# Performance work log

Hardware: AMD Instinct MI355X
Metric: run time of the kernel (lower is better)

Reference implementation:

```python
import jax, jax.numpy as jnp
import numpy as np

N, B, E, H, D, L, NT = 30000, 16, 60000, 128, 64, 2, 5


def _build_graph():
    rng = np.random.default_rng(0)
    ng = N // B
    row = rng.integers(0, N, size=E)
    g = row // ng
    col = g * ng + rng.integers(0, ng, size=E)  # bonds stay within a graph
    order = np.argsort(g, kind='stable')        # sort bonds by graph id
    row, col = row[order], col[order]
    edge_index = np.stack([row, col]).astype(np.int32)
    # bond graph: bonds adjacent iff they share an atom (vectorized _build_bond_graph)
    atoms = np.concatenate([row, col])
    bonds = np.concatenate([np.arange(E), np.arange(E)])
    o2 = np.argsort(atoms, kind='stable')
    sb = bonds[o2]
    counts = np.bincount(atoms, minlength=N)
    offs = np.concatenate([[0], np.cumsum(counts)[:-1]])
    sq = counts * counts
    total = int(sq.sum())
    gid = np.repeat(np.arange(N), sq)
    poff = np.concatenate([[0], np.cumsum(sq)[:-1]])
    pos = np.arange(total) - np.repeat(poff, sq)
    c, o = counts[gid], offs[gid]
    ii, jj = pos // c, pos % c
    mask = ii != jj
    bond_edge_index = np.stack([sb[o + ii][mask], sb[o + jj][mask]]).astype(np.int32)
    batch = np.repeat(np.arange(B), ng).astype(np.int32)
    return edge_index, bond_edge_index, batch


def setup_inputs() -> dict:
    edge_index, bond_edge_index, batch = _build_graph()
    key = jax.random.key(0)
    ks = jax.random.split(key, 16)
    s = 0.05
    n = lambda k, shp: jax.random.normal(k, shp, jnp.float32) * s
    return {
        'atom_features': jax.random.normal(ks[0], (N, H), jnp.float32),
        'atom_pos': jax.random.normal(ks[1], (N, 3), jnp.float32),
        'atomic_numbers': jax.random.randint(ks[2], (N,), 1, 20, jnp.int32),
        'batch': jnp.asarray(batch),
        'edge_index': jnp.asarray(edge_index),
        'bond_edge_index': jnp.asarray(bond_edge_index),
        'iw1': n(ks[3], (2 * H, D)), 'ib1': jnp.zeros((D,), jnp.float32),
        'iw2': n(ks[4], (D, D)), 'ib2': jnp.zeros((D,), jnp.float32),
        'emb': n(ks[5], (L, NT, D)),
        'mw1': n(ks[6], (L, 3 * D, D)), 'mb1': jnp.zeros((L, D), jnp.float32),
        'mw2': n(ks[7], (L, D, D)), 'mb2': jnp.zeros((L, D), jnp.float32),
        'uw1': n(ks[8], (L, 2 * D, D)), 'ub1': jnp.zeros((L, D), jnp.float32),
        'uw2': n(ks[9], (L, D, D)), 'ub2': jnp.zeros((L, D), jnp.float32),
        'num_graphs': B,
    }


def reference(atom_features, atom_pos, iw1, ib1, iw2, ib2, emb, mw1, mb1, mw2, mb2,
              uw1, ub1, uw2, ub2, atomic_numbers, batch, edge_index, bond_edge_index,
              num_graphs):
    row, col = edge_index
    hi, hj = atom_features[row], atom_features[col]  # [E, H] gathers
    # bond_init MLP
    x = jax.nn.silu(jnp.concatenate([hi, hj], -1) @ iw1 + ib1) @ iw2 + ib2  # [E, D]
    # _classify_bonds: cosine-similarity thresholds (order matters, matches torch)
    ni = jnp.maximum(jnp.linalg.norm(hi, axis=-1), 1e-8)
    nj = jnp.maximum(jnp.linalg.norm(hj, axis=-1), 1e-8)
    sim = jnp.sum(hi * hj, -1) / (ni * nj)
    bt = jnp.where(sim > 0.8, 1, 0)
    bt = jnp.where(sim > 0.9, 2, bt)
    bt = jnp.where(sim < 0.3, 3, bt)
    src, dst = bond_edge_index  # x_j = x[src], x_i = x[dst]; aggregate at dst
    nb = x.shape[0]
    deg = jax.ops.segment_sum(jnp.ones(src.shape, jnp.float32), dst, num_segments=nb)
    denom = jnp.maximum(deg, 1.0)[:, None]  # PyG mean aggr: 0 for isolated nodes
    for l in range(mw1.shape[0]):
        te = emb[l][bt]  # [E, D] bond-type embedding
        msg_in = jnp.concatenate([x[dst], x[src], te[dst]], -1)  # [BE, 3D]
        msg = jax.nn.silu(msg_in @ mw1[l] + mb1[l]) @ mw2[l] + mb2[l]
        aggr = jax.ops.segment_sum(msg, dst, num_segments=nb) / denom
        upd_in = jnp.concatenate([aggr, x], -1)
        x = x + jax.nn.silu(upd_in @ uw1[l] + ub1[l]) @ uw2[l] + ub2[l]
    # pooling: edges are sorted by graph, so repeat_interleave == batch[row]
    bond_batch = batch[row]
    cnt = jax.ops.segment_sum(jnp.ones((nb,), jnp.float32), bond_batch, num_segments=num_graphs)
    gfeat = jax.ops.segment_sum(x, bond_batch, num_segments=num_graphs) / jnp.maximum(cnt, 1.0)[:, None]
    return x, gfeat
```

## Files before the change

### kernel.cpp

```cpp
#include <hip/hip_runtime.h>
#include <cstdint>
#include <cstddef>

#define HDIM 128
#define DDIM 64
#define NTYPES 5
#define NGRAPHS 16
#define EPB 64
#define SCAP 1024

typedef __attribute__((ext_vector_type(8))) short short8;
typedef __attribute__((ext_vector_type(4))) float f32x4;

static __device__ __forceinline__ short8 as_s8(uint4 u) {
    return __builtin_bit_cast(short8, u);
}

static __device__ __forceinline__ float silu_f(float v) {
    return v * __builtin_amdgcn_rcpf(1.0f + __expf(-v));
}

static __device__ __forceinline__ float4 ld4(const float* p) {
    return *reinterpret_cast<const float4*>(p);
}

static __device__ __forceinline__ void st4(float* p, float4 v) {
    *reinterpret_cast<float4*>(p) = v;
}

static __device__ __forceinline__ float4 add4(float4 a, float4 b) {
    return make_float4(a.x + b.x, a.y + b.y, a.z + b.z, a.w + b.w);
}
// ... 26 lines not shown
    a.x = __uint_as_float(u.x << 16);
    a.y = __uint_as_float(u.x & 0xFFFF0000u);
    a.z = __uint_as_float(u.y << 16);
    a.w = __uint_as_float(u.y & 0xFFFF0000u);
    b.x = __uint_as_float(u.z << 16);
    b.y = __uint_as_float(u.z & 0xFFFF0000u);
    b.z = __uint_as_float(u.w << 16);
    b.w = __uint_as_float(u.w & 0xFFFF0000u);
}

static __device__ __forceinline__ void hilo8(const float* f, uint4& h, uint4& lo) {
    h = pack8(f);
    float4 a, b;
    unpack8(h, a, b);
    lo.x = cvtpk(f[0] - a.x, f[1] - a.y);
    lo.y = cvtpk(f[2] - a.z, f[3] - a.w);
    lo.z = cvtpk(f[4] - b.x, f[5] - b.y);
    lo.w = cvtpk(f[6] - b.z, f[7] - b.w);
}

static __device__ __forceinline__ int xcd_logical_block() {
    int chunk = (int)(gridDim.x >> 3);
    return (int)(blockIdx.x & 7) * chunk + (int)(blockIdx.x >> 3);
}

__global__ void __launch_bounds__(256) count_k(const int* __restrict__ bdst,
                                               int* __restrict__ cnt, int BE) {
    int i = blockIdx.x * 256 + threadIdx.x;
    if (i < BE)
        __hip_atomic_fetch_add(&cnt[bdst[i]], 1, __ATOMIC_RELAXED, __HIP_MEMORY_SCOPE_AGENT);
}

__global__ void __launch_bounds__(256) bsum_k(const int* __restrict__ cnt,
                                              int* __restrict__ bsum, int E) {
    __shared__ int red[256];
    int t = threadIdx.x;
    int i = blockIdx.x * 256 + t;
    red[t] = (i < E) ? cnt[i] : 0;
    __syncthreads();
    #pragma unroll
    for (int off = 128; off > 0; off >>= 1) {
        if (t < off) red[t] += red[t + off];
        __syncthreads();
    }
    if (t == 0) bsum[blockIdx.x] = red[0];
}

__global__ void __launch_bounds__(1024) bscan_k(const int* __restrict__ bsum,
                                                int* __restrict__ bpre, int NB) {
    __shared__ int sh[1024];
    int t = threadIdx.x;
    int v0 = (t < NB) ? bsum[t] : 0;
    sh[t] = v0;
// ... 21 lines not shown
        int v = (t >= off) ? sh[t - off] : 0;
        __syncthreads();
        sh[t] += v;
        __syncthreads();
    }
    int ex = sh[t] - v0 + bpre[blockIdx.x];
    if (i < E) { offs[i] = ex; cursor[i] = ex; }
    if (i == E - 1) offs[E] = ex + v0;
}

__global__ void __launch_bounds__(256) scatter_k(const int* __restrict__ bsrc,
                                                 const int* __restrict__ bdst,
                                                 int* __restrict__ cursor,
                                                 int* __restrict__ srclist, int BE) {
    int i = blockIdx.x * 256 + threadIdx.x;
    if (i < BE) {
        int d = bdst[i];
        int p = __hip_atomic_fetch_add(&cursor[d], 1, __ATOMIC_RELAXED,
                                       __HIP_MEMORY_SCOPE_AGENT);
        srclist[p] = bsrc[i];
    }
}

__global__ void __launch_bounds__(64) prep_k(const float* __restrict__ emb,
                                             const float* __restrict__ mw1,
                                             const float* __restrict__ mb1,
                                             const float* __restrict__ mw2,
                                             const float* __restrict__ mb2,
                                             const float* __restrict__ uw1,
                                             const float* __restrict__ uw2,
                                             const float* __restrict__ iw2,
                                             const float* __restrict__ iw1,
                                             float* __restrict__ tt,
                                             float* __restrict__ b2u,
                                             uint4* __restrict__ fw2u,
                                             uint4* __restrict__ fu1b,
                                             uint4* __restrict__ fu2,
                                             uint4* __restrict__ fp,
                                             uint4* __restrict__ fiw2,
                                             uint4* __restrict__ fp0,
                                             uint4* __restrict__ fiw1) {
    int b = blockIdx.x;
    int l = threadIdx.x;
    if (b < 10) {
        int ll = b / NTYPES, t = b % NTYPES;
        const float* embl = emb + (size_t)ll * NTYPES * DDIM + (size_t)t * DDIM;
        const float* w1 = mw1 + (size_t)ll * 192 * DDIM;
        float s = mb1[ll * DDIM + l];
        #pragma unroll 8
        for (int k = 0; k < DDIM; ++k)
            s = fmaf(embl[k], w1[(HDIM + k) * DDIM + l], s);
        tt[(size_t)b * DDIM + l] = s;
        return;
    }
    if (b < 12) {
        int ll = b - 10;
        const float* u1 = uw1 + (size_t)ll * 128 * DDIM;
        float s = 0.f;
        #pragma unroll 8
        for (int t = 0; t < DDIM; ++t)
            s = fmaf(mb2[ll * DDIM + t], u1[(size_t)t * DDIM + l], s);
        b2u[ll * DDIM + l] = s;
        return;
    }
    int pb = b - 12;
    int mat = pb >> 3, jt = (pb >> 1) & 3, ks = pb & 1;
// ... 20 lines not shown
            case 3:  src = uw1 + 128 * 64 + 64 * 64;         dst = fu1b + 1024; break;
            case 4:  src = uw2;                              dst = fu2;         break;
            case 5:  src = uw2 + 4096;                       dst = fu2 + 1024;  break;
            case 6:  src = mw1 + (size_t)192 * 64;           dst = fp;          break;
            case 7:  src = mw1 + (size_t)192 * 64 + 64 * 64; dst = fp + 1024;   break;
            case 8:  src = iw2;                              dst = fiw2;        break;
            case 9:  src = mw1;                              dst = fp0;         break;
            case 10: src = mw1 + (size_t)64 * 64;            dst = fp0 + 1024;  break;
            case 11: src = iw1;                              dst = fiw1;        break;
            case 12: src = iw1 + (size_t)64 * 64;            dst = fiw1 + 1024; break;
            case 13: src = iw1 + (size_t)128 * 64;           dst = fiw1 + 2048; break;
            default: src = iw1 + (size_t)192 * 64;           dst = fiw1 + 3072; break;
        }
        #pragma unroll
        for (int i = 0; i < 8; ++i) f[i] = src[(size_t)(k0 + i) * DDIM + j];
    }
    uint4 h, lo;
    hilo8(f, h, lo);
    size_t di = ((size_t)(jt * 2 + ks) * 64 + l) * 2;
    dst[di] = h;
    dst[di + 1] = lo;
}

static __device__ __forceinline__ int slotIdx(int row, int slot) {
    return row * 8 + (slot ^ (row & 7));
}
static __device__ __forceinline__ int slotIdx16(int row, int slot) {
    return row * 16 + (slot ^ (row & 7));
}

static __device__ __forceinline__ short8 ldFragA(const uint4* buf, int rowBase, int lane, int ks) {
    int row = rowBase + (lane & 15);
    int slot = ks * 4 + (lane >> 4);
    return as_s8(buf[slotIdx(row, slot)]);
}
static __device__ __forceinline__ short8 ldFragA16(const uint4* buf, int rowBase, int lane, int slot0) {
    int row = rowBase + (lane & 15);
    int slot = slot0 + (lane >> 4);
    return as_s8(buf[slotIdx16(row, slot)]);
}

static __device__ __forceinline__ void loadB(const uint4* __restrict__ frag, int jt, int lane,
                                             short8& h0, short8& h1, short8& l0, short8& l1) {
    const uint4* p0 = frag + ((size_t)(jt * 2 + 0) * 64 + lane) * 2;
    const uint4* p1 = frag + ((size_t)(jt * 2 + 1) * 64 + lane) * 2;
    h0 = as_s8(p0[0]); l0 = as_s8(p0[1]);
// ... 12 lines not shown
    acc = __builtin_amdgcn_mfma_f32_16x16x32_bf16(al0, bh0, acc, 0, 0, 0);
    acc = __builtin_amdgcn_mfma_f32_16x16x32_bf16(al1, bh1, acc, 0, 0, 0);
    acc = __builtin_amdgcn_mfma_f32_16x16x32_bf16(ah0, bl0, acc, 0, 0, 0);
    acc = __builtin_amdgcn_mfma_f32_16x16x32_bf16(ah1, bl1, acc, 0, 0, 0);
    return acc;
}

static __device__ __forceinline__ f32x4 gemm_tile16(const uint4* Ahi, const uint4* Alo,
        int rowBase, int lane, int sb,
        short8 bh0, short8 bh1, short8 bl0, short8 bl1, f32x4 acc) {
    short8 ah0 = ldFragA16(Ahi, rowBase, lane, sb + 0);
    short8 ah1 = ldFragA16(Ahi, rowBase, lane, sb + 4);
    short8 al0 = ldFragA16(Alo, rowBase, lane, sb + 0);
    short8 al1 = ldFragA16(Alo, rowBase, lane, sb + 4);
    acc = __builtin_amdgcn_mfma_f32_16x16x32_bf16(ah0, bh0, acc, 0, 0, 0);
    acc = __builtin_amdgcn_mfma_f32_16x16x32_bf16(ah1, bh1, acc, 0, 0, 0);
    acc = __builtin_amdgcn_mfma_f32_16x16x32_bf16(al0, bh0, acc, 0, 0, 0);
    acc = __builtin_amdgcn_mfma_f32_16x16x32_bf16(al1, bh1, acc, 0, 0, 0);
    acc = __builtin_amdgcn_mfma_f32_16x16x32_bf16(ah0, bl0, acc, 0, 0, 0);
    acc = __builtin_amdgcn_mfma_f32_16x16x32_bf16(ah1, bl1, acc, 0, 0, 0);
    return acc;
}

__global__ void __launch_bounds__(512) atom_proj_k(
    const float* __restrict__ AF, const uint4* __restrict__ fIw1,
    float* __restrict__ pa, float* __restrict__ qa, float* __restrict__ na, int N) {
    __shared__ uint4 sHi[1024];
    __shared__ uint4 sLo[1024];
    int tid = threadIdx.x;
    int lane = tid & 63;
    int w = __builtin_amdgcn_readfirstlane((int)(tid >> 6));
    int a0 = blockIdx.x * 64;

    {
        int dl = tid >> 3, q = tid & 7;
        int a = a0 + dl;
        bool ok = a < N;
        const float* ar = AF + (size_t)(ok ? a : 0) * HDIM + q * 16;
        float4 v0 = ld4(ar + 0), v1 = ld4(ar + 4), v2 = ld4(ar + 8), v3 = ld4(ar + 12);
        float nrm = v0.x*v0.x + v0.y*v0.y + v0.z*v0.z + v0.w*v0.w
                  + v1.x*v1.x + v1.y*v1.y + v1.z*v1.z + v1.w*v1.w
                  + v2.x*v2.x + v2.y*v2.y + v2.z*v2.z + v2.w*v2.w
                  + v3.x*v3.x + v3.y*v3.y + v3.z*v3.z + v3.w*v3.w;
        nrm += __shfl_xor(nrm, 1, 64);
        nrm += __shfl_xor(nrm, 2, 64);
        nrm += __shfl_xor(nrm, 4, 64);
        if (q == 0 && ok) na[a] = sqrtf(nrm);
        float f0[8] = {v0.x, v0.y, v0.z, v0.w, v1.x, v1.y, v1.z, v1.w};
        float f1[8] = {v2.x, v2.y, v2.z, v2.w, v3.x, v3.y, v3.z, v3.w};
        if (!ok) {
            #pragma unroll
            for (int i = 0; i < 8; ++i) { f0[i] = 0.f; f1[i] = 0.f; }
        }
        uint4 h, l;
        hilo8(f0, h, l);
        int s0 = slotIdx16(dl, q * 2);
// ... 5 lines not shown
    int jt = w & 3;
    const uint4* m0 = fIw1 + ((w < 4) ? 0 : 2048);
    short8 B0h0, B0h1, B0l0, B0l1, B1h0, B1h1, B1l0, B1l1;
    loadB(m0, jt, lane, B0h0, B0h1, B0l0, B0l1);
    loadB(m0 + 1024, jt, lane, B1h0, B1h1, B1l0, B1l1);
    __syncthreads();

    float* dst = (w < 4) ? pa : qa;
    int j = jt * 16 + (lane & 15);
    f32x4 z4 = {0.f, 0.f, 0.f, 0.f};
    #pragma unroll
    for (int rt = 0; rt < 4; ++rt) {
        f32x4 acc = gemm_tile16(sHi, sLo, rt * 16, lane, 0, B0h0, B0h1, B0l0, B0l1, z4);
        acc = gemm_tile16(sHi, sLo, rt * 16, lane, 8, B1h0, B1h1, B1l0, B1l1, acc);
        #pragma unroll
        for (int r = 0; r < 4; ++r) {
            int rowi = rt * 16 + (lane >> 4) * 4 + r;
            int a = a0 + rowi;
            if (a < N) dst[(size_t)a * DDIM + j] = acc[r];
        }
    }
}

__global__ void __launch_bounds__(512, 4) bond_init2_k(
    const float* __restrict__ AF, const int* __restrict__ row, const int* __restrict__ col,
    const float* __restrict__ pa, const float* __restrict__ qa, const float* __restrict__ na,
    const float* __restrict__ b1, const uint4* __restrict__ fW2, const float* __restrict__ b2,
    const uint4* __restrict__ fP0,
    float* __restrict__ x, int* __restrict__ bt,
    float* __restrict__ pd, uint4* __restrict__ ps, int E) {
    __shared__ uint4 sAhi[512];
    __shared__ uint4 sAlo[512];
    __shared__ uint4 sXhi[512];
    __shared__ uint4 sXlo[512];
    int nEB = (E + EPB - 1) / EPB;
    int lb = xcd_logical_block();
    if (lb >= nEB) return;
    int tid = threadIdx.x;
    int lane = tid & 63;
    int w = __builtin_amdgcn_readfirstlane((int)(tid >> 6));
    int e0 = lb * EPB;

    {
        int dl = tid >> 3, q = tid & 7;
        int d = e0 + dl;
        bool ok = d < E;
        int dd = ok ? d : 0;
        int r = row[dd], c = col[dd];
        int jq = q * 8;

        const float* hi = AF + (size_t)r * HDIM + q * 16;
        const float* hj = AF + (size_t)c * HDIM + q * 16;
        float dt = 0.f;
        #pragma unroll
        for (int k = 0; k < 16; k += 4) {
            float4 a4 = ld4(hi + k), b4 = ld4(hj + k);
            dt += a4.x * b4.x + a4.y * b4.y + a4.z * b4.z + a4.w * b4.w;
        }
        dt += __shfl_xor(dt, 1, 64);
        dt += __shfl_xor(dt, 2, 64);
        dt += __shfl_xor(dt, 4, 64);
        if (q == 0 && ok) {
            float nr = fmaxf(na[r], 1e-8f), nc = fmaxf(na[c], 1e-8f);
// ... 25 lines not shown
        uint4 h4, l4;
        hilo8(hv, h4, l4);
        int si = slotIdx(dl, q);
        sAhi[si] = h4; sAlo[si] = l4;
    }
    int jt = w & 3, mh = w >> 2;
    short8 W2h0, W2h1, W2l0, W2l1;
    loadB(fW2, jt, lane, W2h0, W2h1, W2l0, W2l1);
    __syncthreads();

    int rb0 = mh * 32, rb1 = mh * 32 + 16;
    f32x4 z4 = {0.f, 0.f, 0.f, 0.f};
    f32x4 acc0 = gemm_tile(sAhi, sAlo, rb0, lane, W2h0, W2h1, W2l0, W2l1, z4);
    f32x4 acc1 = gemm_tile(sAhi, sAlo, rb1, lane, W2h0, W2h1, W2l0, W2l1, z4);
    int j = jt * 16 + (lane & 15);
    float b2j = b2[j];
    unsigned short* hX = (unsigned short*)sXhi;
    unsigned short* lX = (unsigned short*)sXlo;
    #pragma unroll
    for (int r = 0; r < 4; ++r) {
        int rowi = rb0 + (lane >> 4) * 4 + r;
        int e = e0 + rowi;
        float xn = acc0[r] + b2j;
        if (e < E) x[(size_t)e * DDIM + j] = xn;
        unsigned int hb = bf16r(xn);
        float lov = xn - __uint_as_float(hb << 16);
        int ui = (rowi * 8 + ((j >> 3) ^ (rowi & 7))) * 8 + (j & 7);
        hX[ui] = (unsigned short)hb;
        lX[ui] = (unsigned short)bf16r(lov);
    }
    #pragma unroll
    for (int r = 0; r < 4; ++r) {
        int rowi = rb1 + (lane >> 4) * 4 + r;
        int e = e0 + rowi;
        float xn = acc1[r] + b2j;
        if (e < E) x[(size_t)e * DDIM + j] = xn;
        unsigned int hb = bf16r(xn);
        float lov = xn - __uint_as_float(hb << 16);
        int ui = (rowi * 8 + ((j >> 3) ^ (rowi & 7))) * 8 + (j & 7);
        hX[ui] = (unsigned short)hb;
        lX[ui] = (unsigned short)bf16r(lov);
    }
    __syncthreads();

    const uint4* fPw = (w < 4) ? fP0 : (fP0 + 1024);
    int jp = w & 3;
    short8 Ph0, Ph1, Pl0, Pl1;
    loadB(fPw, jp, lane, Ph0, Ph1, Pl0, Pl1);
    f32x4 q0 = gemm_tile(sXhi, sXlo, 0,  lane, Ph0, Ph1, Pl0, Pl1, z4);
    f32x4 q1 = gemm_tile(sXhi, sXlo, 16, lane, Ph0, Ph1, Pl0, Pl1, z4);
    f32x4 q2 = gemm_tile(sXhi, sXlo, 32, lane, Ph0, Ph1, Pl0, Pl1, z4);
    f32x4 q3 = gemm_tile(sXhi, sXlo, 48, lane, Ph0, Ph1, Pl0, Pl1, z4);
    unsigned short* hA = (unsigned short*)sAhi;
    if (w < 4) {
        int jd = jp * 16 + (lane & 15);
        #pragma unroll
        for (int mt = 0; mt < 4; ++mt) {
            f32x4 qq = (mt == 0) ? q0 : (mt == 1) ? q1 : (mt == 2) ? q2 : q3;
            #pragma unroll
// ... 4 lines not shown
            }
        }
    } else {
        int js = jp * 16 + (lane & 15);
        #pragma unroll
        for (int mt = 0; mt < 4; ++mt) {
            f32x4 qq = (mt == 0) ? q0 : (mt == 1) ? q1 : (mt == 2) ? q2 : q3;
            #pragma unroll
            for (int r = 0; r < 4; ++r) {
                int rowi = mt * 16 + (lane >> 4) * 4 + r;
                int ui = (rowi * 8 + ((js >> 3) ^ (rowi & 7))) * 8 + (js & 7);
                hA[ui] = (unsigned short)bf16r(qq[r]);
            }
        }
    }
    __syncthreads();
    {
        int dl = tid >> 3, q = tid & 7;
        int d = e0 + dl;
        if (d < E) ps[(size_t)d * 8 + q] = sAhi[slotIdx(dl, q)];
    }
}

__global__ void __launch_bounds__(256) proj_k(const float* __restrict__ x,
                                              const float* __restrict__ w1 ,
                                              float* __restrict__ pd, uint4* __restrict__ ps,
                                              int E) {
    int lane = threadIdx.x & 63;
    int w = __builtin_amdgcn_readfirstlane((int)(threadIdx.x >> 6));
    int e = blockIdx.x * EPB + lane;
    bool ok = e < E;
    int eidx = ok ? e : 0;
    int j0 = w * 16;
    const float* xr = x + (size_t)eidx * DDIM;

    float apd[16], aps[16];
    #pragma unroll
    for (int jj = 0; jj < 16; ++jj) { apd[jj] = 0.f; aps[jj] = 0.f; }
    #pragma unroll 2
    for (int c = 0; c < 16; ++c) {
        float4 v = ld4(xr + c * 4);
        float xv[4] = {v.x, v.y, v.z, v.w};
        #pragma unroll
        for (int kk = 0; kk < 4; ++kk) {
            int k = c * 4 + kk;
            const float* wd = w1 + (size_t)k * DDIM + j0;
            const float* wsv = w1 + (size_t)(DDIM + k) * DDIM + j0;
            #pragma unroll
            for (int jj = 0; jj < 16; ++jj) {
                apd[jj] = fmaf(xv[kk], wd[jj], apd[jj]);
                aps[jj] = fmaf(xv[kk], wsv[jj], aps[jj]);
            }
        }
    }
    if (ok) {
        float* pr = pd + (size_t)e * DDIM + j0;
        st4(pr + 0,  make_float4(apd[0],  apd[1],  apd[2],  apd[3]));
        st4(pr + 4,  make_float4(apd[4],  apd[5],  apd[6],  apd[7]));
        st4(pr + 8,  make_float4(apd[8],  apd[9],  apd[10], apd[11]));
        st4(pr + 12, make_float4(apd[12], apd[13], apd[14], apd[15]));
        ps[(size_t)e * 8 + 2 * w + 0] = pack8(aps + 0);
        ps[(size_t)e * 8 + 2 * w + 1] = pack8(aps + 8);
    }
}

__global__ void __launch_bounds__(512, 4) layer_k(
    float* __restrict__ x, const float* __restrict__ pd, const uint4* __restrict__ ps,
    const float* __restrict__ tt_l, const int* __restrict__ bt,
    const int* __restrict__ offs, const int* __restrict__ srclist,
    const int* __restrict__ cnt,
    const uint4* __restrict__ fW2u, const float* __restrict__ b2u,
    const uint4* __restrict__ fU1b, const float* __restrict__ ub1,
    const uint4* __restrict__ fU2, const float* __restrict__ ub2,
    const uint4* __restrict__ fP ,
    float* __restrict__ pdn, uint4* __restrict__ psn, int E,
    const int* __restrict__ erow, const int* __restrict__ gbatch,
    float* __restrict__ gfeat, int doPool) {
    __shared__ uint4 sAhi[512];
    __shared__ uint4 sAlo[512];
    __shared__ uint4 sXhi[512];
    __shared__ uint4 sXlo[512];
    __shared__ float degLDS[64];
    __shared__ int   gidLDS[64];
    __shared__ int   sIdx[SCAP];
    int nEB = (E + EPB - 1) / EPB;
    int lb = xcd_logical_block();
    if (lb >= nEB) return;
    int tid = threadIdx.x;
    int lane = tid & 63;
    int w = __builtin_amdgcn_readfirstlane((int)(tid >> 6));
    int e0 = lb * EPB;
    int pb0 = offs[e0];

    {
        int dl = tid >> 3, q = tid & 7;
        int d = e0 + dl;
        bool ok = d < E;
        int dd = ok ? d : 0;
        int jq = q * 8;
        const float* xr = x + (size_t)dd * DDIM + jq;
        float4 xv0 = ld4(xr + 0), xv1 = ld4(xr + 4);
        int dc = cnt[dd];
        int rAtom = (doPool && ok) ? erow[dd] : 0;
        const float* pr = pd + (size_t)dd * DDIM + jq;
        const float* tp = tt_l + (size_t)bt[dd] * DDIM + jq;
        float4 b0 = add4(ld4(pr + 0), ld4(tp + 0));
        float4 b1 = add4(ld4(pr + 4), ld4(tp + 4));
        int p0v = ok ? offs[d] : pb0, p1v = ok ? offs[d + 1] : pb0;

        int emax = min(e0 + EPB, E);
        int pT = offs[emax] - pb0;
        for (int i = tid; i < pT && i < SCAP; i += 512) sIdx[i] = srclist[pb0 + i];
        __syncthreads();

        float4 s0 = make_float4(0, 0, 0, 0), s1 = s0;
        if (p1v - pb0 <= SCAP) {
            int li = p0v - pb0, le = p1v - pb0;
            for (; li + 4 <= le; li += 4) {
                uint4 u0 = ps[(size_t)sIdx[li + 0] * 8 + q];
                uint4 u1 = ps[(size_t)sIdx[li + 1] * 8 + q];
                uint4 u2 = ps[(size_t)sIdx[li + 2] * 8 + q];
                uint4 u3 = ps[(size_t)sIdx[li + 3] * 8 + q];
                float4 a, b;
                unpack8(u0, a, b);
// ... 28 lines not shown
                silu_acc4(s0, add4(b0, a));
                silu_acc4(s1, add4(b1, b));
                unpack8(u1, a, b);
                silu_acc4(s0, add4(b0, a));
                silu_acc4(s1, add4(b1, b));
                unpack8(u2, a, b);
                silu_acc4(s0, add4(b0, a));
                silu_acc4(s1, add4(b1, b));
                unpack8(u3, a, b);
                silu_acc4(s0, add4(b0, a));
                silu_acc4(s1, add4(b1, b));
            }
            for (; p < p1v; ++p) {
                uint4 u0 = ps[(size_t)srclist[p] * 8 + q];
                float4 a, b;
                unpack8(u0, a, b);
                silu_acc4(s0, add4(b0, a));
                silu_acc4(s1, add4(b1, b));
            }
        }
        float inv = 1.0f / fmaxf((float)dc, 1.0f);
        float sv[8] = {s0.x * inv, s0.y * inv, s0.z * inv, s0.w * inv,
                       s1.x * inv, s1.y * inv, s1.z * inv, s1.w * inv};
        float xf[8] = {xv0.x, xv0.y, xv0.z, xv0.w, xv1.x, xv1.y, xv1.z, xv1.w};
        if (!ok) {
            #pragma unroll
            for (int i = 0; i < 8; ++i) { sv[i] = 0.f; xf[i] = 0.f; }
        }
        uint4 h4, l4;
        int si = slotIdx(dl, q);
        hilo8(sv, h4, l4);
        sAhi[si] = h4; sAlo[si] = l4;
        hilo8(xf, h4, l4);
        sXhi[si] = h4; sXlo[si] = l4;
        if (q == 0) {
            degLDS[dl] = (ok && dc > 0) ? 1.0f : 0.0f;
            gidLDS[dl] = (doPool && ok) ? gbatch[rAtom] : -1;
        }
    }
    int jt = w & 3, mh = w >> 2;
    short8 A2h0, A2h1, A2l0, A2l1;
    short8 U1h0, U1h1, U1l0, U1l1;
    loadB(fW2u, jt, lane, A2h0, A2h1, A2l0, A2l1);
    loadB(fU1b, jt, lane, U1h0, U1h1, U1l0, U1l1);
    __syncthreads();

    int rb0 = mh * 32, rb1 = mh * 32 + 16;
    f32x4 z4 = {0.f, 0.f, 0.f, 0.f};
    f32x4 acc0 = z4, acc1 = z4;
    acc0 = gemm_tile(sAhi, sAlo, rb0, lane, A2h0, A2h1, A2l0, A2l1, acc0);
    acc0 = gemm_tile(sXhi, sXlo, rb0, lane, U1h0, U1h1, U1l0, U1l1, acc0);
    acc1 = gemm_tile(sAhi, sAlo, rb1, lane, A2h0, A2h1, A2l0, A2l1, acc1);
    acc1 = gemm_tile(sXhi, sXlo, rb1, lane, U1h0, U1h1, U1l0, U1l1, acc1);
    __syncthreads();
    int j = jt * 16 + (lane & 15);
    float ub1j = ub1[j], b2uj = b2u[j];
    unsigned short* hA = (unsigned short*)sAhi;
// ... 18 lines not shown
        hA[ui] = (unsigned short)hb;
        lA[ui] = (unsigned short)bf16r(lov);
    }
    __syncthreads();

    short8 U2h0, U2h1, U2l0, U2l1;
    loadB(fU2, jt, lane, U2h0, U2h1, U2l0, U2l1);
    f32x4 o0 = gemm_tile(sAhi, sAlo, rb0, lane, U2h0, U2h1, U2l0, U2l1, z4);
    f32x4 o1 = gemm_tile(sAhi, sAlo, rb1, lane, U2h0, U2h1, U2l0, U2l1, z4);
    float ub2j = ub2[j];
    bool haveP = (fP != nullptr);
    unsigned short* hX = (unsigned short*)sXhi;
    unsigned short* lX = (unsigned short*)sXlo;
    float xnv0[4], xnv1[4];
    #pragma unroll
    for (int r = 0; r < 4; ++r) {
        int row = rb0 + (lane >> 4) * 4 + r;
        int e = e0 + row;
        int ui = (row * 8 + ((j >> 3) ^ (row & 7))) * 8 + (j & 7);
        float xvv = __uint_as_float((unsigned int)hX[ui] << 16)
                  + __uint_as_float((unsigned int)lX[ui] << 16);
        float xn = xvv + o0[r] + ub2j;
        xnv0[r] = xn;
        if (e < E) x[(size_t)e * DDIM + j] = xn;
        if (haveP) {
            unsigned int hb = bf16r(xn);
            float lov = xn - __uint_as_float(hb << 16);
            hX[ui] = (unsigned short)hb;
            lX[ui] = (unsigned short)bf16r(lov);
        }
    }
    #pragma unroll
    for (int r = 0; r < 4; ++r) {
        int row = rb1 + (lane >> 4) * 4 + r;
        int e = e0 + row;
        int ui = (row * 8 + ((j >> 3) ^ (row & 7))) * 8 + (j & 7);
        float xvv = __uint_as_float((unsigned int)hX[ui] << 16)
                  + __uint_as_float((unsigned int)lX[ui] << 16);
        float xn = xvv + o1[r] + ub2j;
        xnv1[r] = xn;
        if (e < E) x[(size_t)e * DDIM + j] = xn;
        if (haveP) {
            unsigned int hb = bf16r(xn);
            float lov = xn - __uint_as_float(hb << 16);
            hX[ui] = (unsigned short)hb;
            lX[ui] = (unsigned short)bf16r(lov);
        }
    }
    if (!haveP) {
        if (doPool) {
            __syncthreads();
            float* poolB = (float*)sAhi;
            if (tid < 256) poolB[tid] = 0.f;
            __syncthreads();
            int gid0 = gidLDS[0];
            bool uni = (gidLDS[EPB - 1] == gid0);
            if (uni) {
                float s = xnv0[0] + xnv0[1] + xnv0[2] + xnv0[3]
                        + xnv1[0] + xnv1[1] + xnv1[2] + xnv1[3];
                atomicAdd(&poolB[j], s);
            } else {
                #pragma unroll
                for (int r = 0; r < 4; ++r) {
                    int row = rb0 + (lane >> 4) * 4 + r;
// ... 49 lines not shown
            }
        }
    } else {
        int js = jp * 16 + (lane & 15);
        #pragma unroll
        for (int mt = 0; mt < 4; ++mt) {
            f32x4 qq = (mt == 0) ? q0 : (mt == 1) ? q1 : (mt == 2) ? q2 : q3;
            #pragma unroll
            for (int r = 0; r < 4; ++r) {
                int row = mt * 16 + (lane >> 4) * 4 + r;
                int ui = (row * 8 + ((js >> 3) ^ (row & 7))) * 8 + (js & 7);
                hA[ui] = (unsigned short)bf16r(qq[r]);
            }
        }
    }
    __syncthreads();
    {
        int dl = tid >> 3, q = tid & 7;
        int d = e0 + dl;
        if (d < E) psn[(size_t)d * 8 + q] = sAhi[slotIdx(dl, q)];
    }
}

static __device__ __forceinline__ int lower_bound_bb(const int* __restrict__ row,
                                                     const int* __restrict__ batch,
                                                     int E, int g) {
    int lo = 0, hi = E;
    while (lo < hi) {
        int m = (lo + hi) >> 1;
        if (batch[row[m]] < g) lo = m + 1; else hi = m;
    }
    return lo;
}

__global__ void __launch_bounds__(64) pool_final_k(
    const int* __restrict__ row, const int* __restrict__ batch,
    float* __restrict__ gfeat, int E) {
    int g = blockIdx.x, j = threadIdx.x;
    int s = lower_bound_bb(row, batch, E, g);
    int t = lower_bound_bb(row, batch, E, g + 1);
    float cnt = fmaxf((float)(t - s), 1.0f);
    gfeat[g * DDIM + j] /= cnt;
}

extern "C" void kernel_launch(void* const* d_in, const int* in_sizes, int n_in,
                              void* d_out, int out_size, void* d_ws, size_t ws_size,
                              hipStream_t stream) {
    (void)n_in; (void)out_size;
    const float* AF    = (const float*)d_in[0];
    const int*   batch = (const int*)d_in[3];
    const int*   edge_index      = (const int*)d_in[4];
    const int*   bond_edge_index = (const int*)d_in[5];
    const float* iw1 = (const float*)d_in[6];
    const float* ib1 = (const float*)d_in[7];
    const float* iw2 = (const float*)d_in[8];
    const float* ib2 = (const float*)d_in[9];
    const float* emb = (const float*)d_in[10];
    const float* mw1 = (const float*)d_in[11];
    const float* mb1 = (const float*)d_in[12];
    const float* mw2 = (const float*)d_in[13];
    const float* mb2 = (const float*)d_in[14];
    const float* uw1 = (const float*)d_in[15];
    const float* ub1 = (const float*)d_in[16];
    const float* uw2 = (const float*)d_in[17];
    const float* ub2 = (const float*)d_in[18];

    const int N  = in_sizes[0] / HDIM;
    const int E  = in_sizes[4] / 2;
    const int BE = in_sizes[5] / 2;
    const int NB = (E + 255) / 256;
    const int EB = (E + EPB - 1) / EPB;
    const int APB = (N + 63) / 64;
    const int EBS = ((EB + 7) / 8) * 8;

    float* xout  = (float*)d_out;
    float* gfeat = xout + (size_t)E * DDIM;

    char* w = (char*)d_ws;
    float* tt       = (float*)w;  w += sizeof(float) * 2 * NTYPES * DDIM;
    float* b2u      = (float*)w;  w += sizeof(float) * 2 * DDIM;
    w = (char*)(((uintptr_t)w + 15) & ~(uintptr_t)15);
    uint4* fW2u     = (uint4*)w;  w += 2048 * sizeof(uint4);
    uint4* fU1b     = (uint4*)w;  w += 2048 * sizeof(uint4);
    uint4* fU2      = (uint4*)w;  w += 2048 * sizeof(uint4);
    uint4* fP       = (uint4*)w;  w += 2048 * sizeof(uint4);
    uint4* fIw2     = (uint4*)w;  w += 1024 * sizeof(uint4);
    uint4* fP0      = (uint4*)w;  w += 2048 * sizeof(uint4);
    uint4* fIw1     = (uint4*)w;  w += 4096 * sizeof(uint4);
    int*   cnt      = (int*)w;    w += sizeof(int) * E;
    int*   offs     = (int*)w;    w += sizeof(int) * (E + 1);
    int*   cursor   = (int*)w;    w += sizeof(int) * E;
    int*   bt       = (int*)w;    w += sizeof(int) * E;
    int*   bsum     = (int*)w;    w += sizeof(int) * 1024;
    int*   bpre     = (int*)w;    w += sizeof(int) * 1024;
    int*   srclist  = (int*)w;    w += sizeof(int) * BE;
    w = (char*)(((uintptr_t)w + 15) & ~(uintptr_t)15);
    float* pd       = (float*)w;  w += sizeof(float) * (size_t)E * DDIM;
    uint4* ps       = (uint4*)w;  w += sizeof(unsigned short) * (size_t)E * DDIM;
    float* pa       = (float*)w;  w += sizeof(float) * (size_t)N * DDIM;
    float* qa       = (float*)w;  w += sizeof(float) * (size_t)N * DDIM;
    float* na       = (float*)w;  w += sizeof(float) * (size_t)N;
    w = (char*)(((uintptr_t)w + 15) & ~(uintptr_t)15);
    float* pd2      = (float*)w;  w += sizeof(float) * (size_t)E * DDIM;
    uint4* ps2      = (uint4*)w;  w += sizeof(unsigned short) * (size_t)E * DDIM;
    bool fuse_proj = ((size_t)(w - (char*)d_ws) <= ws_size);

    const int* row  = edge_index;
    const int* col  = edge_index + E;
    const int* bsrc = bond_edge_index;
    const int* bdst = bond_edge_index + BE;

    hipMemsetAsync(cnt, 0, (size_t)E * sizeof(int), stream);
    count_k<<<(BE + 255) / 256, 256, 0, stream>>>(bdst, cnt, BE);
    bsum_k<<<NB, 256, 0, stream>>>(cnt, bsum, E);
    bscan_k<<<1, 1024, 0, stream>>>(bsum, bpre, NB);
    offs_k<<<NB, 256, 0, stream>>>(cnt, bpre, offs, cursor, E);
    scatter_k<<<(BE + 255) / 256, 256, 0, stream>>>(bsrc, bdst, cursor, srclist, BE);

    prep_k<<<132, 64, 0, stream>>>(emb, mw1, mb1, mw2, mb2, uw1, uw2, iw2, iw1,
                                   tt, b2u, fW2u, fU1b, fU2, fP, fIw2, fP0, fIw1);

    atom_proj_k<<<APB, 512, 0, stream>>>(AF, fIw1, pa, qa, na, N);
    bond_init2_k<<<EBS, 512, 0, stream>>>(AF, row, col, pa, qa, na, ib1, fIw2, ib2,
                                          fP0, xout, bt, pd, ps, E);

    hipMemsetAsync(gfeat, 0, NGRAPHS * DDIM * sizeof(float), stream);

    if (fuse_proj) {
        layer_k<<<EBS, 512, 0, stream>>>(
            xout, pd, ps, tt, bt, offs, srclist, cnt,
            fW2u, b2u, fU1b, ub1, fU2, ub2,
            fP, pd2, ps2, E, row, batch, gfeat, 0);
        layer_k<<<EBS, 512, 0, stream>>>(
            xout, pd2, ps2, tt + NTYPES * DDIM, bt, offs, srclist, cnt,
            fW2u + 1024, b2u + DDIM, fU1b + 1024, ub1 + DDIM,
            fU2 + 1024, ub2 + DDIM,
            nullptr, nullptr, nullptr, E, row, batch, gfeat, 1);
    } else {
        for (int l = 0; l < 2; ++l) {
            if (l > 0)
                proj_k<<<EB, 256, 0, stream>>>(xout, mw1 + (size_t)l * 192 * 64, pd, ps, E);
            layer_k<<<EBS, 512, 0, stream>>>(
                xout, pd, ps, tt + (size_t)l * NTYPES * DDIM, bt, offs, srclist, cnt,
                fW2u + (size_t)l * 1024, b2u + (size_t)l * DDIM,
                fU1b + (size_t)l * 1024, ub1 + (size_t)l * DDIM,
                fU2 + (size_t)l * 1024, ub2 + (size_t)l * DDIM,
                nullptr, nullptr, nullptr, E, row, batch, gfeat, l == 1 ? 1 : 0);
        }
    }

    pool_final_k<<<NGRAPHS, 64, 0, stream>>>(row, batch, gfeat, E);
}
```

Before: 285.3 us.

## Fuse atom projection, bond init and both layers into one cooperative kernel

Replaces the chain of atom_proj, bond_init, two layer kernels, gfeat memset and pool_final launches with one cooperative kernel that uses grid-wide syncs between stages. Intermediate x stores and reloads are skipped because x is already held in LDS across stages. The prep and count kernels are also merged into a single launch. The aim is to cut launch gaps and some global traffic. In exchange it adds grid.sync costs, requires the whole grid to be co-resident (there is a fallback path), and caps occupancy through the launch bounds.

```diff
diff --git a/kernel.cpp b/kernel.cpp
--- a/kernel.cpp
+++ b/kernel.cpp
@@ -1,6 +1,9 @@
 #include <hip/hip_runtime.h>
+#include <hip/hip_cooperative_groups.h>
 #include <cstdint>
 #include <cstddef>
+
+namespace cg = cooperative_groups;
 
 #define HDIM 128
 #define DDIM 64
@@ -8,6 +11,7 @@
 #define NGRAPHS 16
 #define EPB 64
 #define SCAP 1024
+#define PREPB 132
 
 typedef __attribute__((ext_vector_type(8))) short short8;
 typedef __attribute__((ext_vector_type(4))) float f32x4;
@@ -80,13 +84,6 @@
 static __device__ __forceinline__ int xcd_logical_block() {
     int chunk = (int)(gridDim.x >> 3);
     return (int)(blockIdx.x & 7) * chunk + (int)(blockIdx.x >> 3);
-}
-
-__global__ void __launch_bounds__(256) count_k(const int* __restrict__ bdst,
-                                               int* __restrict__ cnt, int BE) {
-    int i = blockIdx.x * 256 + threadIdx.x;
-    if (i < BE)
-        __hip_atomic_fetch_add(&cnt[bdst[i]], 1, __ATOMIC_RELAXED, __HIP_MEMORY_SCOPE_AGENT);
 }
 
 __global__ void __launch_bounds__(256) bsum_k(const int* __restrict__ cnt,
@@ -154,26 +151,25 @@
     }
 }
 
-__global__ void __launch_bounds__(64) prep_k(const float* __restrict__ emb,
-                                             const float* __restrict__ mw1,
-                                             const float* __restrict__ mb1,
-                                             const float* __restrict__ mw2,
-                                             const float* __restrict__ mb2,
-                                             const float* __restrict__ uw1,
-                                             const float* __restrict__ uw2,
-                                             const float* __restrict__ iw2,
-                                             const float* __restrict__ iw1,
-                                             float* __restrict__ tt,
-                                             float* __restrict__ b2u,
-                                             uint4* __restrict__ fw2u,
-                                             uint4* __restrict__ fu1b,
-                                             uint4* __restrict__ fu2,
-                                             uint4* __restrict__ fp,
-                                             uint4* __restrict__ fiw2,
-                                             uint4* __restrict__ fp0,
-                                             uint4* __restrict__ fiw1) {
-    int b = blockIdx.x;
-    int l = threadIdx.x;
+static __device__ void dev_prep(int b, int l,
+                                const float* __restrict__ emb,
+                                const float* __restrict__ mw1,
+                                const float* __restrict__ mb1,
+                                const float* __restrict__ mw2,
+                                const float* __restrict__ mb2,
+                                const float* __restrict__ uw1,
+                                const float* __restrict__ uw2,
+                                const float* __restrict__ iw2,
+                                const float* __restrict__ iw1,
+                                float* __restrict__ tt,
+                                float* __restrict__ b2u,
+                                uint4* __restrict__ fw2u,
+                                uint4* __restrict__ fu1b,
+                                uint4* __restrict__ fu2,
+                                uint4* __restrict__ fp,
+                                uint4* __restrict__ fiw2,
+                                uint4* __restrict__ fp0,
+                                uint4* __restrict__ fiw1) {
     if (b < 10) {
         int ll = b / NTYPES, t = b % NTYPES;
         const float* embl = emb + (size_t)ll * NTYPES * DDIM + (size_t)t * DDIM;
@@ -240,6 +236,29 @@
     dst[di + 1] = lo;
 }
 
+__global__ void __launch_bounds__(256) prepcount_k(
+    const float* __restrict__ emb, const float* __restrict__ mw1,
+    const float* __restrict__ mb1, const float* __restrict__ mw2,
+    const float* __restrict__ mb2, const float* __restrict__ uw1,
+    const float* __restrict__ uw2, const float* __restrict__ iw2,
+    const float* __restrict__ iw1,
+    float* __restrict__ tt, float* __restrict__ b2u,
+    uint4* __restrict__ fw2u, uint4* __restrict__ fu1b, uint4* __restrict__ fu2,
+    uint4* __restrict__ fp, uint4* __restrict__ fiw2, uint4* __restrict__ fp0,
+    uint4* __restrict__ fiw1,
+    const int* __restrict__ bdst, int* __restrict__ cnt, int BE) {
+    int b = blockIdx.x;
+    if (b < PREPB) {
+        if (threadIdx.x < 64)
+            dev_prep(b, threadIdx.x, emb, mw1, mb1, mw2, mb2, uw1, uw2, iw2, iw1,
+                     tt, b2u, fw2u, fu1b, fu2, fp, fiw2, fp0, fiw1);
+        return;
+    }
+    int i = (b - PREPB) * 256 + threadIdx.x;
+    if (i < BE)
+        __hip_atomic_fetch_add(&cnt[bdst[i]], 1, __ATOMIC_RELAXED, __HIP_MEMORY_SCOPE_AGENT);
+}
+
 static __device__ __forceinline__ int slotIdx(int row, int slot) {
     return row * 8 + (slot ^ (row & 7));
 }
@@ -298,16 +317,11 @@
     return acc;
 }
 
-__global__ void __launch_bounds__(512) atom_proj_k(
+static __device__ __forceinline__ void dev_atom_proj(
+    int a0, int tid, int lane, int w,
     const float* __restrict__ AF, const uint4* __restrict__ fIw1,
-    float* __restrict__ pa, float* __restrict__ qa, float* __restrict__ na, int N) {
-    __shared__ uint4 sHi[1024];
-    __shared__ uint4 sLo[1024];
-    int tid = threadIdx.x;
-    int lane = tid & 63;
-    int w = __builtin_amdgcn_readfirstlane((int)(tid >> 6));
-    int a0 = blockIdx.x * 64;
-
+    float* __restrict__ pa, float* __restrict__ qa, float* __restrict__ na, int N,
+    uint4* sHi, uint4* sLo) {
     {
         int dl = tid >> 3, q = tid & 7;
         int a = a0 + dl;
@@ -359,23 +373,27 @@
     }
 }
 
-__global__ void __launch_bounds__(512, 4) bond_init2_k(
+__global__ void __launch_bounds__(512) atom_proj_k(
+    const float* __restrict__ AF, const uint4* __restrict__ fIw1,
+    float* __restrict__ pa, float* __restrict__ qa, float* __restrict__ na, int N) {
+    __shared__ uint4 sHi[1024];
+    __shared__ uint4 sLo[1024];
+    int tid = threadIdx.x, lane = tid & 63;
+    int w = __builtin_amdgcn_readfirstlane((int)(tid >> 6));
+    int a0 = blockIdx.x * 64;
+    if (a0 < N)
+        dev_atom_proj(a0, tid, lane, w, AF, fIw1, pa, qa, na, N, sHi, sLo);
+}
+
+static __device__ __forceinline__ void dev_bond_init(
+    int lb, int tid, int lane, int w,
     const float* __restrict__ AF, const int* __restrict__ row, const int* __restrict__ col,
     const float* __restrict__ pa, const float* __restrict__ qa, const float* __restrict__ na,
     const float* __restrict__ b1, const uint4* __restrict__ fW2, const float* __restrict__ b2,
     const uint4* __restrict__ fP0,
     float* __restrict__ x, int* __restrict__ bt,
-    float* __restrict__ pd, uint4* __restrict__ ps, int E) {
-    __shared__ uint4 sAhi[512];
-    __shared__ uint4 sAlo[512];
-    __shared__ uint4 sXhi[512];
-    __shared__ uint4 sXlo[512];
-    int nEB = (E + EPB - 1) / EPB;
-    int lb = xcd_logical_block();
-    if (lb >= nEB) return;
-    int tid = threadIdx.x;
-    int lane = tid & 63;
-    int w = __builtin_amdgcn_readfirstlane((int)(tid >> 6));
+    float* __restrict__ pd, uint4* __restrict__ ps, int E,
+    uint4* sAhi, uint4* sAlo, uint4* sXhi, uint4* sXlo, bool storeX) {
     int e0 = lb * EPB;
 
     {
@@ -447,7 +465,7 @@
         int rowi = rb0 + (lane >> 4) * 4 + r;
         int e = e0 + rowi;
         float xn = acc0[r] + b2j;
-        if (e < E) x[(size_t)e * DDIM + j] = xn;
+        if (storeX && e < E) x[(size_t)e * DDIM + j] = xn;
         unsigned int hb = bf16r(xn);
         float lov = xn - __uint_as_float(hb << 16);
         int ui = (rowi * 8 + ((j >> 3) ^ (rowi & 7))) * 8 + (j & 7);
@@ -459,7 +477,7 @@
         int rowi = rb1 + (lane >> 4) * 4 + r;
         int e = e0 + rowi;
         float xn = acc1[r] + b2j;
-        if (e < E) x[(size_t)e * DDIM + j] = xn;
+        if (storeX && e < E) x[(size_t)e * DDIM + j] = xn;
         unsigned int hb = bf16r(xn);
         float lov = xn - __uint_as_float(hb << 16);
         int ui = (rowi * 8 + ((j >> 3) ^ (rowi & 7))) * 8 + (j & 7);
@@ -510,6 +528,26 @@
     }
 }
 
+__global__ void __launch_bounds__(512, 4) bond_init2_k(
+    const float* __restrict__ AF, const int* __restrict__ row, const int* __restrict__ col,
+    const float* __restrict__ pa, const float* __restrict__ qa, const float* __restrict__ na,
+    const float* __restrict__ b1, const uint4* __restrict__ fW2, const float* __restrict__ b2,
+    const uint4* __restrict__ fP0,
+    float* __restrict__ x, int* __restrict__ bt,
+    float* __restrict__ pd, uint4* __restrict__ ps, int E) {
+    __shared__ uint4 sAhi[512];
+    __shared__ uint4 sAlo[512];
+    __shared__ uint4 sXhi[512];
+    __shared__ uint4 sXlo[512];
+    int nEB = (E + EPB - 1) / EPB;
+    int lb = xcd_logical_block();
+    if (lb >= nEB) return;
+    int tid = threadIdx.x, lane = tid & 63;
+    int w = __builtin_amdgcn_readfirstlane((int)(tid >> 6));
+    dev_bond_init(lb, tid, lane, w, AF, row, col, pa, qa, na, b1, fW2, b2, fP0,
+                  x, bt, pd, ps, E, sAhi, sAlo, sXhi, sXlo, true);
+}
+
 __global__ void __launch_bounds__(256) proj_k(const float* __restrict__ x,
                                               const float* __restrict__ w1 ,
                                               float* __restrict__ pd, uint4* __restrict__ ps,
@@ -552,7 +590,8 @@
     }
 }
 
-__global__ void __launch_bounds__(512, 4) layer_k(
+static __device__ __forceinline__ void dev_layer(
+    int lb, int tid, int lane, int w,
     float* __restrict__ x, const float* __restrict__ pd, const uint4* __restrict__ ps,
     const float* __restrict__ tt_l, const int* __restrict__ bt,
     const int* __restrict__ offs, const int* __restrict__ srclist,
@@ -560,23 +599,11 @@
     const uint4* __restrict__ fW2u, const float* __restrict__ b2u,
     const uint4* __restrict__ fU1b, const float* __restrict__ ub1,
     const uint4* __restrict__ fU2, const float* __restrict__ ub2,
-    const uint4* __restrict__ fP ,
-    float* __restrict__ pdn, uint4* __restrict__ psn, int E,
-    const int* __restrict__ erow, const int* __restrict__ gbatch,
-    float* __restrict__ gfeat, int doPool) {
-    __shared__ uint4 sAhi[512];
-    __shared__ uint4 sAlo[512];
-    __shared__ uint4 sXhi[512];
-    __shared__ uint4 sXlo[512];
-    __shared__ float degLDS[64];
-    __shared__ int   gidLDS[64];
-    __shared__ int   sIdx[SCAP];
-    int nEB = (E + EPB - 1) / EPB;
-    int lb = xcd_logical_block();
-    if (lb >= nEB) return;
-    int tid = threadIdx.x;
-    int lane = tid & 63;
-    int w = __builtin_amdgcn_readfirstlane((int)(tid >> 6));
+    const uint4* __restrict__ fP, float* __restrict__ pdn, uint4* __restrict__ psn,
+    int E, const int* __restrict__ erow, const int* __restrict__ gbatch,
+    float* __restrict__ gfeat, int doPool,
+    uint4* sAhi, uint4* sAlo, uint4* sXhi, uint4* sXlo,
+    float* degLDS, int* gidLDS, int* sIdx, bool loadX, bool storeX3) {
     int e0 = lb * EPB;
     int pb0 = offs[e0];
 
@@ -586,8 +613,11 @@
         bool ok = d < E;
         int dd = ok ? d : 0;
         int jq = q * 8;
-        const float* xr = x + (size_t)dd * DDIM + jq;
-        float4 xv0 = ld4(xr + 0), xv1 = ld4(xr + 4);
+        float4 xv0 = make_float4(0, 0, 0, 0), xv1 = xv0;
+        if (loadX) {
+            const float* xr = x + (size_t)dd * DDIM + jq;
+            xv0 = ld4(xr + 0); xv1 = ld4(xr + 4);
+        }
         int dc = cnt[dd];
         int rAtom = (doPool && ok) ? erow[dd] : 0;
         const float* pr = pd + (size_t)dd * DDIM + jq;
@@ -662,17 +692,23 @@
         float inv = 1.0f / fmaxf((float)dc, 1.0f);
         float sv[8] = {s0.x * inv, s0.y * inv, s0.z * inv, s0.w * inv,
                        s1.x * inv, s1.y * inv, s1.z * inv, s1.w * inv};
-        float xf[8] = {xv0.x, xv0.y, xv0.z, xv0.w, xv1.x, xv1.y, xv1.z, xv1.w};
         if (!ok) {
             #pragma unroll
-            for (int i = 0; i < 8; ++i) { sv[i] = 0.f; xf[i] = 0.f; }
+            for (int i = 0; i < 8; ++i) sv[i] = 0.f;
         }
         uint4 h4, l4;
         int si = slotIdx(dl, q);
         hilo8(sv, h4, l4);
         sAhi[si] = h4; sAlo[si] = l4;
-        hilo8(xf, h4, l4);
-        sXhi[si] = h4; sXlo[si] = l4;
+        if (loadX) {
+            float xf[8] = {xv0.x, xv0.y, xv0.z, xv0.w, xv1.x, xv1.y, xv1.z, xv1.w};
+            if (!ok) {
+                #pragma unroll
+                for (int i = 0; i < 8; ++i) xf[i] = 0.f;
+            }
+            hilo8(xf, h4, l4);
+            sXhi[si] = h4; sXlo[si] = l4;
+        }
         if (q == 0) {
             degLDS[dl] = (ok && dc > 0) ? 1.0f : 0.0f;
             gidLDS[dl] = (doPool && ok) ? gbatch[rAtom] : -1;
@@ -737,7 +773,7 @@
                   + __uint_as_float((unsigned int)lX[ui] << 16);
         float xn = xvv + o0[r] + ub2j;
         xnv0[r] = xn;
-        if (e < E) x[(size_t)e * DDIM + j] = xn;
+        if (storeX3 && e < E) x[(size_t)e * DDIM + j] = xn;
         if (haveP) {
             unsigned int hb = bf16r(xn);
             float lov = xn - __uint_as_float(hb << 16);
@@ -754,7 +790,7 @@
                   + __uint_as_float((unsigned int)lX[ui] << 16);
         float xn = xvv + o1[r] + ub2j;
         xnv1[r] = xn;
-        if (e < E) x[(size_t)e * DDIM + j] = xn;
+        if (storeX3 && e < E) x[(size_t)e * DDIM + j] = xn;
         if (haveP) {
             unsigned int hb = bf16r(xn);
             float lov = xn - __uint_as_float(hb << 16);
@@ -850,6 +886,36 @@
     }
 }
 
+__global__ void __launch_bounds__(512, 4) layer_k(
+    float* __restrict__ x, const float* __restrict__ pd, const uint4* __restrict__ ps,
+    const float* __restrict__ tt_l, const int* __restrict__ bt,
+    const int* __restrict__ offs, const int* __restrict__ srclist,
+    const int* __restrict__ cnt,
+    const uint4* __restrict__ fW2u, const float* __restrict__ b2u,
+    const uint4* __restrict__ fU1b, const float* __restrict__ ub1,
+    const uint4* __restrict__ fU2, const float* __restrict__ ub2,
+    const uint4* __restrict__ fP,
+    float* __restrict__ pdn, uint4* __restrict__ psn, int E,
+    const int* __restrict__ erow, const int* __restrict__ gbatch,
+    float* __restrict__ gfeat, int doPool) {
+    __shared__ uint4 sAhi[512];
+    __shared__ uint4 sAlo[512];
+    __shared__ uint4 sXhi[512];
+    __shared__ uint4 sXlo[512];
+    __shared__ float degLDS[64];
+    __shared__ int   gidLDS[64];
+    __shared__ int   sIdx[SCAP];
+    int nEB = (E + EPB - 1) / EPB;
+    int lb = xcd_logical_block();
+    if (lb >= nEB) return;
+    int tid = threadIdx.x, lane = tid & 63;
+    int w = __builtin_amdgcn_readfirstlane((int)(tid >> 6));
+    dev_layer(lb, tid, lane, w, x, pd, ps, tt_l, bt, offs, srclist, cnt,
+              fW2u, b2u, fU1b, ub1, fU2, ub2, fP, pdn, psn, E,
+              erow, gbatch, gfeat, doPool,
+              sAhi, sAlo, sXhi, sXlo, degLDS, gidLDS, sIdx, true, true);
+}
+
 static __device__ __forceinline__ int lower_bound_bb(const int* __restrict__ row,
                                                      const int* __restrict__ batch,
                                                      int E, int g) {
@@ -869,6 +935,71 @@
     int t = lower_bound_bb(row, batch, E, g + 1);
     float cnt = fmaxf((float)(t - s), 1.0f);
     gfeat[g * DDIM + j] /= cnt;
+}
+
+__global__ void __launch_bounds__(512, 8) fused_k(
+    float* x, const int* row, const int* col,
+    const float* AF, const uint4* fIw1, float* pa, float* qa, float* na, int N,
+    const float* ib1, const uint4* fIw2, const float* ib2, const uint4* fP0,
+    int* bt, float* pd, uint4* ps,
+    const float* tt, const int* offs, const int* srclist, const int* cnt,
+    const uint4* fW2u, const float* b2u, const uint4* fU1b, const float* ub1,
+    const uint4* fU2, const float* ub2, const uint4* fP,
+    float* pd2, uint4* ps2,
+    const int* gbatch, float* gfeat, int E) {
+    __shared__ uint4 U1[1024];
+    __shared__ uint4 U2[1024];
+    __shared__ float degLDS[64];
+    __shared__ int   gidLDS[64];
+    __shared__ int   sIdx[SCAP];
+    cg::grid_group grid = cg::this_grid();
+    int tid = threadIdx.x, lane = tid & 63;
+    int w = __builtin_amdgcn_readfirstlane((int)(tid >> 6));
+    uint4* sAhi = U1;
+    uint4* sAlo = U1 + 512;
+    uint4* sXhi = U2;
+    uint4* sXlo = U2 + 512;
+
+    if ((int)blockIdx.x * 64 < N)
+        dev_atom_proj((int)blockIdx.x * 64, tid, lane, w, AF, fIw1, pa, qa, na, N, U1, U2);
+    if (blockIdx.x == gridDim.x - 1)
+        for (int i = tid; i < NGRAPHS * DDIM; i += 512) gfeat[i] = 0.f;
+    __threadfence();
+    grid.sync();
+
+    int nEB = (E + EPB - 1) / EPB;
+    int lb = xcd_logical_block();
+
+    if (lb < nEB)
+        dev_bond_init(lb, tid, lane, w, AF, row, col, pa, qa, na, ib1, fIw2, ib2, fP0,
+                      x, bt, pd, ps, E, sAhi, sAlo, sXhi, sXlo, false);
+    __threadfence();
+    grid.sync();
+
+    if (lb < nEB)
+        dev_layer(lb, tid, lane, w, x, pd, ps, tt, bt, offs, srclist, cnt,
+                  fW2u, b2u, fU1b, ub1, fU2, ub2, fP, pd2, ps2, E,
+                  row, gbatch, gfeat, 0,
+                  sAhi, sAlo, sXhi, sXlo, degLDS, gidLDS, sIdx, false, false);
+    __threadfence();
+    grid.sync();
+
+    if (lb < nEB)
+        dev_layer(lb, tid, lane, w, x, pd2, ps2, tt + NTYPES * DDIM, bt, offs, srclist, cnt,
+                  fW2u + 1024, b2u + DDIM, fU1b + 1024, ub1 + DDIM,
+                  fU2 + 1024, ub2 + DDIM, nullptr, nullptr, nullptr, E,
+                  row, gbatch, gfeat, 1,
+                  sAhi, sAlo, sXhi, sXlo, degLDS, gidLDS, sIdx, false, true);
+    __threadfence();
+    grid.sync();
+
+    if ((int)blockIdx.x < NGRAPHS && tid < 64) {
+        int g = blockIdx.x, j = tid;
+        int s = lower_bound_bb(row, gbatch, E, g);
+        int t = lower_bound_bb(row, gbatch, E, g + 1);
+        float c = fmaxf((float)(t - s), 1.0f);
+        gfeat[g * DDIM + j] /= c;
+    }
 }
 
 extern "C" void kernel_launch(void* const* d_in, const int* in_sizes, int n_in,
@@ -900,6 +1031,7 @@
     const int EB = (E + EPB - 1) / EPB;
     const int APB = (N + 63) / 64;
     const int EBS = ((EB + 7) / 8) * 8;
+    const int CNTB = (BE + 255) / 256;
 
     float* xout  = (float*)d_out;
     float* gfeat = xout + (size_t)E * DDIM;
@@ -919,9 +1051,9 @@
     int*   offs     = (int*)w;    w += sizeof(int) * (E + 1);
     int*   cursor   = (int*)w;    w += sizeof(int) * E;
     int*   bt       = (int*)w;    w += sizeof(int) * E;
+    int*   srclist  = (int*)w;    w += sizeof(int) * BE;
     int*   bsum     = (int*)w;    w += sizeof(int) * 1024;
     int*   bpre     = (int*)w;    w += sizeof(int) * 1024;
-    int*   srclist  = (int*)w;    w += sizeof(int) * BE;
     w = (char*)(((uintptr_t)w + 15) & ~(uintptr_t)15);
     float* pd       = (float*)w;  w += sizeof(float) * (size_t)E * DDIM;
     uint4* ps       = (uint4*)w;  w += sizeof(unsigned short) * (size_t)E * DDIM;
@@ -939,43 +1071,72 @@
     const int* bdst = bond_edge_index + BE;
 
     hipMemsetAsync(cnt, 0, (size_t)E * sizeof(int), stream);
-    count_k<<<(BE + 255) / 256, 256, 0, stream>>>(bdst, cnt, BE);
+    prepcount_k<<<PREPB + CNTB, 256, 0, stream>>>(
+        emb, mw1, mb1, mw2, mb2, uw1, uw2, iw2, iw1,
+        tt, b2u, fW2u, fU1b, fU2, fP, fIw2, fP0, fIw1, bdst, cnt, BE);
     bsum_k<<<NB, 256, 0, stream>>>(cnt, bsum, E);
     bscan_k<<<1, 1024, 0, stream>>>(bsum, bpre, NB);
     offs_k<<<NB, 256, 0, stream>>>(cnt, bpre, offs, cursor, E);
     scatter_k<<<(BE + 255) / 256, 256, 0, stream>>>(bsrc, bdst, cursor, srclist, BE);
 
-    prep_k<<<132, 64, 0, stream>>>(emb, mw1, mb1, mw2, mb2, uw1, uw2, iw2, iw1,
-                                   tt, b2u, fW2u, fU1b, fU2, fP, fIw2, fP0, fIw1);
-
-    atom_proj_k<<<APB, 512, 0, stream>>>(AF, fIw1, pa, qa, na, N);
-    bond_init2_k<<<EBS, 512, 0, stream>>>(AF, row, col, pa, qa, na, ib1, fIw2, ib2,
-                                          fP0, xout, bt, pd, ps, E);
-
-    hipMemsetAsync(gfeat, 0, NGRAPHS * DDIM * sizeof(float), stream);
-
-    if (fuse_proj) {
-        layer_k<<<EBS, 512, 0, stream>>>(
-            xout, pd, ps, tt, bt, offs, srclist, cnt,
-            fW2u, b2u, fU1b, ub1, fU2, ub2,
-            fP, pd2, ps2, E, row, batch, gfeat, 0);
-        layer_k<<<EBS, 512, 0, stream>>>(
-            xout, pd2, ps2, tt + NTYPES * DDIM, bt, offs, srclist, cnt,
-            fW2u + 1024, b2u + DDIM, fU1b + 1024, ub1 + DDIM,
-            fU2 + 1024, ub2 + DDIM,
-            nullptr, nullptr, nullptr, E, row, batch, gfeat, 1);
-    } else {
-        for (int l = 0; l < 2; ++l) {
-            if (l > 0)
-                proj_k<<<EB, 256, 0, stream>>>(xout, mw1 + (size_t)l * 192 * 64, pd, ps, E);
+    static int s_coopBlocks = -1;
+    if (s_coopBlocks < 0) {
+        int dev = 0;
+        hipGetDevice(&dev);
+        int coopAttr = 0;
+        hipDeviceGetAttribute(&coopAttr, hipDeviceAttributeCooperativeLaunch, dev);
+        int nCU = 0;
+        hipDeviceGetAttribute(&nCU, hipDeviceAttributeMultiprocessorCount, dev);
+        int mb = 0;
+        hipError_t oe = hipOccupancyMaxActiveBlocksPerMultiprocessor(&mb, fused_k, 512, 0);
+        s_coopBlocks = (coopAttr && oe == hipSuccess && nCU > 0) ? mb * nCU : 0;
+    }
+
+    bool coopDone = false;
+    if (fuse_proj && s_coopBlocks >= EBS) {
+        int Nv = N, Ev = E;
+        void* kargs[] = {
+            (void*)&xout, (void*)&row, (void*)&col,
+            (void*)&AF, (void*)&fIw1, (void*)&pa, (void*)&qa, (void*)&na, (void*)&Nv,
+            (void*)&ib1, (void*)&fIw2, (void*)&ib2, (void*)&fP0,
+            (void*)&bt, (void*)&pd, (void*)&ps,
+            (void*)&tt, (void*)&offs, (void*)&srclist, (void*)&cnt,
+            (void*)&fW2u, (void*)&b2u, (void*)&fU1b, (void*)&ub1,
+            (void*)&fU2, (void*)&ub2, (void*)&fP,
+            (void*)&pd2, (void*)&ps2,
+            (void*)&batch, (void*)&gfeat, (void*)&Ev };
+        hipError_t le = hipLaunchCooperativeKernel((const void*)fused_k, dim3(EBS),
+                                                   dim3(512), kargs, 0, stream);
+        coopDone = (le == hipSuccess);
+    }
+
+    if (!coopDone) {
+        atom_proj_k<<<APB, 512, 0, stream>>>(AF, fIw1, pa, qa, na, N);
+        bond_init2_k<<<EBS, 512, 0, stream>>>(AF, row, col, pa, qa, na, ib1, fIw2, ib2,
+                                              fP0, xout, bt, pd, ps, E);
+        hipMemsetAsync(gfeat, 0, NGRAPHS * DDIM * sizeof(float), stream);
+        if (fuse_proj) {
             layer_k<<<EBS, 512, 0, stream>>>(
-                xout, pd, ps, tt + (size_t)l * NTYPES * DDIM, bt, offs, srclist, cnt,
-                fW2u + (size_t)l * 1024, b2u + (size_t)l * DDIM,
-                fU1b + (size_t)l * 1024, ub1 + (size_t)l * DDIM,
-                fU2 + (size_t)l * 1024, ub2 + (size_t)l * DDIM,
-                nullptr, nullptr, nullptr, E, row, batch, gfeat, l == 1 ? 1 : 0);
-        }
-    }
-
-    pool_final_k<<<NGRAPHS, 64, 0, stream>>>(row, batch, gfeat, E);
-}
+                xout, pd, ps, tt, bt, offs, srclist, cnt,
+                fW2u, b2u, fU1b, ub1, fU2, ub2,
+                fP, pd2, ps2, E, row, batch, gfeat, 0);
+            layer_k<<<EBS, 512, 0, stream>>>(
+                xout, pd2, ps2, tt + NTYPES * DDIM, bt, offs, srclist, cnt,
+                fW2u + 1024, b2u + DDIM, fU1b + 1024, ub1 + DDIM,
+                fU2 + 1024, ub2 + DDIM,
+                nullptr, nullptr, nullptr, E, row, batch, gfeat, 1);
+        } else {
+            for (int l = 0; l < 2; ++l) {
+                if (l > 0)
+                    proj_k<<<EB, 256, 0, stream>>>(xout, mw1 + (size_t)l * 192 * 64, pd, ps, E);
+                layer_k<<<EBS, 512, 0, stream>>>(
+                    xout, pd, ps, tt + (size_t)l * NTYPES * DDIM, bt, offs, srclist, cnt,
+                    fW2u + (size_t)l * 1024, b2u + (size_t)l * DDIM,
+                    fU1b + (size_t)l * 1024, ub1 + (size_t)l * DDIM,
+                    fU2 + (size_t)l * 1024, ub2 + (size_t)l * DDIM,
+                    nullptr, nullptr, nullptr, E, row, batch, gfeat, l == 1 ? 1 : 0);
+            }
+        }
+        pool_final_k<<<NGRAPHS, 64, 0, stream>>>(row, batch, gfeat, E);
+    }
+}
```

Result: no change. 280.0 us, median of 2 (-1.8%).
